# Optimization experiments

Hardware: AMD Instinct MI355X
Metric: run time of the kernel (lower is better)

The kernel has to match this reference:

```python
import jax, jax.numpy as jnp
import numpy as np

LEAK = 0.2

def leaky(x):
    return jnp.where(x > 0, x, LEAK * x)

def relu(x):
    return jnp.maximum(x, 0)

def conv1d(x, w):
    # x [B,Cin,L], w [Cout,Cin,3], stride 1, padding 1
    return jax.lax.conv_general_dilated(x, w, (1,), [(1, 1)],
        dimension_numbers=('NCH', 'OIH', 'NCH'))

def conv2d(x, w, pad, dil=1, groups=1):
    return jax.lax.conv_general_dilated(x, w, (1, 1), [(pad, pad), (pad, pad)],
        rhs_dilation=(dil, dil), feature_group_count=groups,
        dimension_numbers=('NCHW', 'OIHW', 'NCHW'))

def bn2d(x, p, eps=1e-5):
    # p: [4,C] = gamma, beta, running_mean, running_var (eval-mode BN)
    g, b, m, v = p
    s = (1, -1, 1, 1)
    return (x - m.reshape(s)) * (g.reshape(s) / jnp.sqrt(v.reshape(s) + eps)) + b.reshape(s)

def layernorm(x, g, b, eps=1e-5):
    mu = x.mean(-1, keepdims=True)
    var = ((x - mu) ** 2).mean(-1, keepdims=True)
    return (x - mu) / jnp.sqrt(var + eps) * g + b

def l2n(x, axis, eps):
    n = jnp.sqrt((x * x).sum(axis, keepdims=True))
    return x / jnp.maximum(n, eps)


def setup_inputs() -> dict:
    key = jax.random.key(0)
    B, C, H, W = 4, 64, 48, 48
    D, Fn, T, V = 256, 8, 4, 16
    E = 16  # orthogonal prototype embed dim
    ks = iter(jax.random.split(key, 64))
    def rn(shape, s=0.05):
        return jax.random.normal(next(ks), shape, jnp.float32) * s
    def bnp(c):
        return jnp.stack([1.0 + rn((c,), 0.1), rn((c,), 0.1), rn((c,), 0.1), 1.0 + jnp.abs(rn((c,), 0.1))])
    return dict(
        basis_vector_bank=jax.random.normal(next(ks), (T, V, D), jnp.float32),
        task_f=jax.random.normal(next(ks), (B, C, 16, 16), jnp.float32),
        img_f=jax.random.normal(next(ks), (B, C, H, W), jnp.float32),
        protos=jax.random.normal(next(ks), (T, E), jnp.float32),
        tA_w1=rn((E // 4, 1, 3)), tA_w2=rn((E // 2, E // 4, 3)),
        iA_w=rn((E // 2, C, 3, 3)), iA_bn=bnp(E // 2),
        at_w1=rn((E, Fn // 2 * E)), at_b1=rn((Fn // 2 * E,)),
        at_ln_g=jnp.ones((Fn // 2 * E,)), at_ln_b=jnp.zeros((Fn // 2 * E,)),
        at_w2=rn((Fn // 2 * E, Fn * E)), at_b2=rn((Fn * E,)),
        bv_t1=rn((D // 4, 1, 3)), bv_t2=rn((D // 2, D // 4, 3)),
        bv_ic1=rn((D // 4, C, 3, 3)), bv_bn1=bnp(D // 4),
        bv_ic2=rn((D // 2, D // 4, 3, 3)), bv_bn2=bnp(D // 2),
        bv_w1=rn((D, D // 4)), bv_b1=rn((D // 4,)),
        bv_ln_g=jnp.ones((D // 4,)), bv_ln_b=jnp.zeros((D // 4,)),
        bv_w2=rn((D // 4, D)), bv_b2=rn((D,)),
        m1_w1=rn((D, D // 4)), m1_b1=rn((D // 4,)),
        m1_ln_g=jnp.ones((D // 4,)), m1_ln_b=jnp.zeros((D // 4,)),
        m1_w2=rn((D // 4, C * C)), m1_b2=rn((C * C,)),
        m3_w1=rn((D, D // 4)), m3_b1=rn((D // 4,)),
        m3_ln_g=jnp.ones((D // 4,)), m3_ln_b=jnp.zeros((D // 4,)),
        m3_w2=rn((D // 4, 9 * C * C)), m3_b2=rn((9 * C * C,)),
        blr_bn=bnp(C),
        zc_w=rn((C, C, 1, 1), 0.01), zc_b=rn((C,), 0.01),
    )


def _forward(basis_vector_bank, task_f, img_f, protos, tA_w1, tA_w2, iA_w, iA_bn,
             at_w1, at_b1, at_ln_g, at_ln_b, at_w2, at_b2,
             bv_t1, bv_t2, bv_ic1, bv_bn1, bv_ic2, bv_bn2,
             bv_w1, bv_b1, bv_ln_g, bv_ln_b, bv_w2, bv_b2,
             m1_w1, m1_b1, m1_ln_g, m1_ln_b, m1_w2, m1_b2,
             m3_w1, m3_b1, m3_ln_g, m3_ln_b, m3_w2, m3_b2,
             blr_bn, zc_w, zc_b):
    T, V, D = basis_vector_bank.shape
    B, C, H, W = img_f.shape
    E = protos.shape[1]
    Fn = at_w2.shape[1] // E
    tau = 0.5

    # --- A2SI routing features ---
    xt = task_f.reshape(B, 1, -1)
    t1 = conv1d(leaky(conv1d(xt, tA_w1)), tA_w2).mean(-1)          # [B,E/2]
    i1 = leaky(bn2d(conv2d(img_f, iA_w, 1), iA_bn)).mean((2, 3))   # [B,E/2]
    f1 = jnp.concatenate([t1, i1], axis=1)                         # [B,E]
    h = relu(layernorm(f1 @ at_w1 + at_b1, at_ln_g, at_ln_b))
    tif = (h @ at_w2 + at_b2).reshape(B, E, Fn)                    # [B,E,F]
    logits = jnp.einsum('te,bef->bft', l2n(protos, -1, 1e-8), l2n(tif, 1, 1e-8))  # [B,F,T]

    # hard gumbel-softmax (straight-through), fixed noise key for determinism
    u = jax.random.uniform(jax.random.key(42), logits.shape, jnp.float32, 1e-10, 1.0)
    g = -jnp.log(-jnp.log(u))
    y = jax.nn.softmax((logits + g) / tau, axis=-1)
    idx = jnp.argmax(y, axis=-1)                                   # [B,F]
    y_hard = jax.nn.one_hot(idx, T, dtype=y.dtype)
    set_type = y_hard + y - jax.lax.stop_gradient(y)

    bank_flat = basis_vector_bank.reshape(T, V * D)
    sbvb = jnp.einsum('bft,tk->bfk', set_type, bank_flat).reshape(B, Fn, V, D)

    # --- BasisV_filter: filter feature ---
    xt2 = task_f.reshape(B, C, -1)
    rms = jnp.sqrt((xt2 ** 2).mean((1, 2), keepdims=True))
    xt2 = (xt2 / (rms + 1e-8)).reshape(B, 1, -1)
    te = conv1d(leaky(conv1d(xt2, bv_t1)), bv_t2).mean(-1)         # [B,D/2]
    ie = leaky(bn2d(conv2d(img_f, bv_ic1, 1), bv_bn1))
    ie = leaky(bn2d(conv2d(ie, bv_ic2, 1), bv_bn2)).mean((2, 3))   # [B,D/2]
    ff = jnp.concatenate([te, ie], axis=1)                         # [B,D]
    ff = relu(layernorm(ff @ bv_w1 + bv_b1, bv_ln_g, bv_ln_b)) @ bv_w2 + bv_b2

    # --- per-(batch,type) group gather/top-k/scatter, vectorized ---
    # group bank = bank of first filter with that type (hard one-hot -> type's bank)
    occ = idx[:, None, :] == jnp.arange(T)[None, :, None]          # [B,T,F]
    first = jnp.argmax(occ, axis=-1)                               # [B,T]
    Bg = jnp.take_along_axis(sbvb, first[:, :, None, None], axis=1)  # [B,T,V,D]
    # all rows of Q within a group are identical (filter_f expanded over F),
    # so S.max(0) == cosine(ff[b], Bg[b,t])
    scores = jnp.einsum('bd,btvd->btv', l2n(ff, -1, 1e-12), l2n(Bg, -1, 1e-12))
    order = jnp.argsort(-scores, axis=-1)                          # [B,T,V] topk order
    lt = jnp.tril(jnp.ones((Fn, Fn), bool), -1)                    # j < i
    rank = ((idx[:, :, None] == idx[:, None, :]) & lt).sum(-1)     # position in group
    bidx = jnp.arange(B)[:, None]
    sel = order[bidx, idx, rank]                                   # [B,F]
    bvf = Bg[bidx, idx, sel]                                       # [B,F,D]

    # --- per-filter dynamic convolutions ---
    w1 = relu(layernorm(bvf @ m1_w1 + m1_b1, m1_ln_g, m1_ln_b)) @ m1_w2 + m1_b2
    w1 = w1.reshape(B, Fn, C, C)                                   # [B,F,out,in]
    w3 = relu(layernorm(bvf @ m3_w1 + m3_b1, m3_ln_g, m3_ln_b)) @ m3_w2 + m3_b2
    w3 = w3.reshape(B * Fn, C, C, 3, 3)

    dp0 = jnp.einsum('bfoc,bchw->bfohw', w1, img_f)                # 1x1 branch
    xin = jnp.broadcast_to(img_f[:, None], (B, Fn, C, H, W)).reshape(1, B * Fn * C, H, W)
    ker = w3.reshape(B * Fn * C, C, 3, 3)
    dpd = [conv2d(xin, ker, d, dil=d, groups=B * Fn).reshape(B, Fn, C, H, W)
           for d in (1, 2, 3)]                                     # same-padded dilated 3x3
    t_ = idx[:, :, None, None, None]
    dp = jnp.where(t_ == 0, dp0, jnp.where(t_ == 1, dpd[0],
         jnp.where(t_ == 2, dpd[1], dpd[2])))                      # [B,F,C,H,W]

    x = leaky(bn2d(dp.reshape(B * Fn, C, H, W), blr_bn)).reshape(B, Fn, C, H, W).mean(1)
    a = conv2d(x, zc_w, 0) + zc_b.reshape(1, -1, 1, 1)
    return a + img_f


@jax.jit
def reference(basis_vector_bank, task_f, img_f, protos, tA_w1, tA_w2, iA_w, iA_bn,
              at_w1, at_b1, at_ln_g, at_ln_b, at_w2, at_b2,
              bv_t1, bv_t2, bv_ic1, bv_bn1, bv_ic2, bv_bn2,
              bv_w1, bv_b1, bv_ln_g, bv_ln_b, bv_w2, bv_b2,
              m1_w1, m1_b1, m1_ln_g, m1_ln_b, m1_w2, m1_b2,
              m3_w1, m3_b1, m3_ln_g, m3_ln_b, m3_w2, m3_b2,
              blr_bn, zc_w, zc_b):
    return _forward(basis_vector_bank, task_f, img_f, protos, tA_w1, tA_w2, iA_w, iA_bn,
                    at_w1, at_b1, at_ln_g, at_ln_b, at_w2, at_b2,
                    bv_t1, bv_t2, bv_ic1, bv_bn1, bv_ic2, bv_bn2,
                    bv_w1, bv_b1, bv_ln_g, bv_ln_b, bv_w2, bv_b2,
                    m1_w1, m1_b1, m1_ln_g, m1_ln_b, m1_w2, m1_b2,
                    m3_w1, m3_b1, m3_ln_g, m3_ln_b, m3_w2, m3_b2,
                    blr_bn, zc_w, zc_b)
```

## Files before the change

kernel.cpp:

```cpp
#include <hip/hip_runtime.h>
#include <math.h>

#define LEAKC 0.2f

#define NB 4
#define NC 64
#define LLEN 16384
#define HW 2304
#define PP 54
#define PHW 2916
#define SLABP 72
#define CP 72
#define IE1C 50

typedef __attribute__((ext_vector_type(8))) short short8;
typedef __attribute__((ext_vector_type(4))) float floatx4;

__device__ __forceinline__ float leaky(float x){ return x > 0.f ? x : LEAKC*x; }

__device__ __forceinline__ float wave_sum64(float v){
  for(int off=32;off;off>>=1) v += __shfl_xor(v,off);
  return v;
}

__device__ __forceinline__ unsigned short f2bf(float x){
  unsigned u=__float_as_uint(x);
  unsigned r=u+0x7FFFu+((u>>16)&1u);
  return (unsigned short)(r>>16);
}

__device__ __forceinline__ void threefry2x32(unsigned k0, unsigned k1, unsigned& x0, unsigned& x1){
  unsigned ks0=k0, ks1=k1, ks2=k0^k1^0x1BD11BDAu;
  x0+=ks0; x1+=ks1;
  const int rot0[4]={13,15,26,6};
  const int rot1[4]={17,29,16,24};
#define TF_APPLY(rr) {for(int r=0;r<4;r++){x0+=x1; x1=(x1<<rr[r])|(x1>>(32-rr[r])); x1^=x0;}}
  TF_APPLY(rot0); x0+=ks1; x1+=ks2+1u;
  TF_APPLY(rot1); x0+=ks2; x1+=ks0+2u;
  TF_APPLY(rot0); x0+=ks0; x1+=ks1+3u;
  TF_APPLY(rot1); x0+=ks1; x1+=ks2+4u;
  TF_APPLY(rot0); x0+=ks2; x1+=ks0+5u;
#undef TF_APPLY
}

__device__ __forceinline__ float jax_uniform128(int i){
  unsigned x0=0u, x1=(unsigned)i;
  threefry2x32(0u,42u,x0,x1);
  unsigned bits = x0 ^ x1;
  unsigned fb=(bits>>9)|0x3f800000u;
  float f=__uint_as_float(fb)-1.0f;
  float u=f*(1.0f-1e-10f)+1e-10f;
  return fmaxf(1e-10f,u);
}

struct MidSM {
  float sT[64], s0[64], sL[64];
  float red8[64][9];
  float totA_s[4]; float rms_s;
  float part[512];
  float te_s[128], t1_s[8];
  float f1[16], h[64], tif[128], tifn[128], tden[8], pden[4], pn[64], z[32];
  int sidx[8], sfirst[4], srank[8], rows[8];
  float fbuf[256], hh[64], ffn_s[256], finv_s;
  float scores[64];
  int order[64];
  float bvf[2048];
};

__global__ __launch_bounds__(256) void k_pre(const float* __restrict__ task_f,
                      const float* __restrict__ w1A, const float* __restrict__ w1B,
                      float* __restrict__ totApart, float* __restrict__ a0A, float* __restrict__ aLA,
                      float* __restrict__ totBpart, float* __restrict__ a0B, float* __restrict__ aLB,
                      float* __restrict__ rmspart,
                      const float* __restrict__ img,
                      const float* __restrict__ w1, const float* __restrict__ w2,
                      const float* __restrict__ wa,
                      unsigned short* __restrict__ imgTP,
                      unsigned short* __restrict__ W1T, unsigned short* __restrict__ W2T,
                      unsigned short* __restrict__ WAT,
                      const float* __restrict__ mw1, const float* __restrict__ mw3,
                      const float* __restrict__ bvw1p, const float* __restrict__ bvw2p,
                      const float* __restrict__ bvt2p, const float* __restrict__ atw2p,
                      const float* __restrict__ bankp,
                      const float* __restrict__ m1w2p, const float* __restrict__ m3w2p,
                      const float* __restrict__ zcwp,
                      float* __restrict__ warm, int* __restrict__ cnt){
  if(blockIdx.x<256){
    int b=blockIdx.x>>6, seg=blockIdx.x&63;
    const float* x=task_f+b*LLEN;
    float tA[4]={0,0,0,0};
    float tB[64];
#pragma unroll
    for(int c=0;c<64;c++) tB[c]=0.f;
    float sq=0.f;
    int l=seg*256+threadIdx.x;
    {
      float xm=(l>0)?x[l-1]:0.f;
      float xc=x[l];
      float xp=(l<LLEN-1)?x[l+1]:0.f;
      sq=xc*xc;
#pragma unroll
      for(int c=0;c<4;c++){
        float a=leaky(w1A[c*3+0]*xm + w1A[c*3+1]*xc + w1A[c*3+2]*xp);
        tA[c]=a;
        if(l==0) a0A[b*4+c]=a;
        if(l==LLEN-1) aLA[b*4+c]=a;
      }
#pragma unroll
      for(int c=0;c<64;c++){
        float a=leaky(w1B[c*3+0]*xm + w1B[c*3+1]*xc + w1B[c*3+2]*xp);
        tB[c]=a;
        if(l==0) a0B[b*64+c]=a;
        if(l==LLEN-1) aLB[b*64+c]=a;
      }
    }
    sq=wave_sum64(sq);
#pragma unroll
    for(int c=0;c<4;c++) tA[c]=wave_sum64(tA[c]);
#pragma unroll
    for(int c=0;c<64;c++){
      float v=tB[c];
      for(int off=32;off;off>>=1) v+=__shfl_down(v,off);
      tB[c]=v;
    }
    __shared__ float redB[4][64];
    __shared__ float redA[4][4];
    __shared__ float redQ[4];
    int wave=threadIdx.x>>6, lane=threadIdx.x&63;
    if(lane==0){
#pragma unroll
      for(int c=0;c<64;c++) redB[wave][c]=tB[c];
#pragma unroll
      for(int c=0;c<4;c++) redA[wave][c]=tA[c];
      redQ[wave]=sq;
    }
    __syncthreads();
    if(threadIdx.x<64){
      float s=redB[0][threadIdx.x]+redB[1][threadIdx.x]+redB[2][threadIdx.x]+redB[3][threadIdx.x];
      totBpart[(size_t)(b*64+seg)*64+threadIdx.x]=s;
    } else if(threadIdx.x<68){
      int c=threadIdx.x-64;
      totApart[(b*64+seg)*4+c]=redA[0][c]+redA[1][c]+redA[2][c]+redA[3][c];
    } else if(threadIdx.x==68){
      rmspart[b*64+seg]=redQ[0]+redQ[1]+redQ[2]+redQ[3];
    }
  } else if(blockIdx.x<400){
    int blk=blockIdx.x-256;
    int b=blk/36, t=blk%36;
    int p0=t*64;
    __shared__ float tile[64][65];
    int pp=threadIdx.x&63, c4=threadIdx.x>>6;
    for(int r=0;r<16;r++){
      int c=c4*16+r;
      tile[c][pp]=img[(b*64+c)*HW + p0+pp];
    }
    __syncthreads();
    int pxl=threadIdx.x>>2, cg=(threadIdx.x&3)*16;
    unsigned out[8];
#pragma unroll
    for(int q=0;q<8;q++){
      unsigned lo=f2bf(tile[cg+2*q][pxl]);
      unsigned hi=f2bf(tile[cg+2*q+1][pxl]);
      out[q]=lo|(hi<<16);
    }
    int px=p0+pxl;
    int h=px/48, w=px-h*48;
    int poff=(h+3)*PP+(w+3);
    unsigned* dst=(unsigned*)(imgTP + ((size_t)(b*PHW+poff))*64 + cg);
#pragma unroll
    for(int q=0;q<8;q++) dst[q]=out[q];
  } else if(blockIdx.x<868){
    int n=(blockIdx.x-400)*256+threadIdx.x;
    if(n<9*64*64){
      int tap=n>>12, oc=(n>>6)&63, c=n&63;
      W1T[n]=f2bf(w1[oc*576+c*9+tap]);
    } else if(n<9*64*64+9*128*64){
      int m=n-9*64*64;
      int tap=m/8192, r=m-tap*8192, oc=r>>6, c=r&63;
      W2T[m]=f2bf(w2[oc*576+c*9+tap]);
    } else {
      int q=n-9*64*64-9*128*64;
      if(q<9*16*64){
        int tap=q>>10, r=q&1023, o=r>>6, c=r&63;
        WAT[q]=(o<8)?f2bf(wa[o*576+c*9+tap]):(unsigned short)0;
      }
    }
  } else if(blockIdx.x<932){
    int t=(blockIdx.x-868)*256+threadIdx.x;
    float a=0.f;
    for(int i=t;i*16<16384;i+=16384) a+=mw1[i*16];
    for(int i=t;i*16<16384;i+=16384) a+=mw3[i*16];
    for(int i=t;i*16<16384;i+=16384) a+=bvw1p[i*16];
    for(int i=t;i*16<16384;i+=16384) a+=bvw2p[i*16];
    for(int i=t;i*16<24576;i+=16384) a+=bvt2p[i*16];
    for(int i=t;i*16<8192;i+=16384) a+=atw2p[i*16];
    for(int i=t;i*16<16384;i+=16384) a+=bankp[i*16];
    for(int i=t;i*16<262144;i+=16384) a+=m1w2p[i*16];
    for(int i=t;i*16<2359296;i+=16384) a+=m3w2p[i*16];
    for(int i=t;i*16<4096;i+=16384) a+=zcwp[i*16];
    warm[t&1023]=a;
  } else {
    if(blockIdx.x==932 && threadIdx.x<4)
      __hip_atomic_store(&cnt[threadIdx.x],0,__ATOMIC_RELAXED,__HIP_MEMORY_SCOPE_AGENT);
    int id=(blockIdx.x-932)*256+threadIdx.x;
    uint4 z=make_uint4(0,0,0,0);
    for(int cch=id;cch<19584;cch+=4096){
      int ck=cch&7, pxid=cch>>3;
      int b=pxid/612, p=pxid-b*612;
      int h,w;
      if(p<324){ int r=p/54; w=p-r*54; h=(r<3)?r:(r+48); }
      else { int q=p-324; int r2=q/6; int cc=q-r2*6; h=3+r2; w=(cc<3)?cc:(cc+48); }
      *(uint4*)(imgTP + ((size_t)(b*PHW + h*PP + w))*64 + ck*8)=z;
    }
  }
}

__global__ __launch_bounds__(512) void k_cm(const unsigned short* __restrict__ imgTP,
    const unsigned short* __restrict__ W1T, const unsigned short* __restrict__ W2T,
    const unsigned short* __restrict__ WAT,
    const float* __restrict__ bn1, const float* __restrict__ bn2, const float* __restrict__ bnA,
    float* __restrict__ iepart, float* __restrict__ i1part,
    const float* __restrict__ totApart, const float* __restrict__ a0A, const float* __restrict__ aLA,
    const float* __restrict__ totBpart, const float* __restrict__ a0B, const float* __restrict__ aLB,
    const float* __restrict__ rmspart,
    const float* __restrict__ tA_w2, const float* __restrict__ bv_t2,
    const float* __restrict__ at_w1, const float* __restrict__ at_b1,
    const float* __restrict__ at_ln_g, const float* __restrict__ at_ln_b,
    const float* __restrict__ at_w2, const float* __restrict__ at_b2,
    const float* __restrict__ protos,
    const float* __restrict__ bv_w1, const float* __restrict__ bv_b1,
    const float* __restrict__ bv_ln_g, const float* __restrict__ bv_ln_b,
    const float* __restrict__ bv_w2, const float* __restrict__ bv_b2,
    const float* __restrict__ bank,
    const float* __restrict__ m1_w1, const float* __restrict__ m1_b1,
    const float* __restrict__ m1_g,  const float* __restrict__ m1_bb,
    const float* __restrict__ m3_w1, const float* __restrict__ m3_b1,
    const float* __restrict__ m3_g,  const float* __restrict__ m3_bb,
    int* __restrict__ idxo, float* __restrict__ hid1, float* __restrict__ hid3,
    int* __restrict__ cnt){
  __shared__ __align__(16) char smraw[75456];
  int tid=threadIdx.x;
  int lane=tid&63, wv=tid>>6;
  int n0=lane&15, kg=lane>>4;
  if(blockIdx.x<96){
    int blk=blockIdx.x;
    int b=blk/24, hp=blk-b*24;
    int h0=hp*2;
    unsigned short* slab=(unsigned short*)smraw;
    unsigned short* ie1=(unsigned short*)(smraw+46656);
    {
      const unsigned short* ibase=imgTP+((size_t)b*PHW+(size_t)(h0+1)*PP)*64;
      for(int e=tid;e<6*54*8;e+=512){
        int rr=e/(54*8), rem=e-rr*54*8, w=rem>>3, ck=rem&7;
        uint4 v=*(const uint4*)(ibase+((size_t)(rr*PP+w))*64+ck*8);
        *(uint4*)(slab+(rr*54+w)*SLABP+ck*8)=v;
      }
      if(tid<64){
        int br=tid>>4, cq=(tid>>3)&1, ck=tid&7;
        *(uint4*)(ie1+((size_t)(br*IE1C+(cq?49:0)))*CP+ck*8)=make_uint4(0,0,0,0);
      }
    }
    __syncthreads();
    {
      int mt=wv&3, rh=wv>>2;
      floatx4 acc[2][3];
#pragma unroll
      for(int rr=0;rr<2;rr++)
#pragma unroll
        for(int nt=0;nt<3;nt++) acc[rr][nt]=(floatx4){0.f,0.f,0.f,0.f};
#pragma unroll
      for(int ti=0;ti<3;ti++){
#pragma unroll
        for(int tj=0;tj<3;tj++){
          int tap=ti*3+tj;
          const unsigned short* Ab=W1T+(size_t)tap*4096;
#pragma unroll
          for(int c0=0;c0<64;c0+=32){
            short8 a=*(const short8*)(Ab+((mt*16+n0)*64+c0+kg*8));
#pragma unroll
            for(int rr=0;rr<2;rr++){
              int sr=rh*2+rr+ti;
#pragma unroll
              for(int nt=0;nt<3;nt++){
                int sc=nt*16+n0+tj+2;
                short8 bv=*(const short8*)(slab+(sr*54+sc)*SLABP+c0+kg*8);
                acc[rr][nt]=__builtin_amdgcn_mfma_f32_16x16x32_bf16(a,bv,acc[rr][nt],0,0,0);
              }
            }
          }
        }
      }
      int obase=mt*16+kg*4;
      float scale[4],m_[4],be_[4];
#pragma unroll
      for(int reg=0;reg<4;reg++){
        int o=obase+reg;
        scale[reg]=bn1[o]/sqrtf(bn1[192+o]+1e-5f);
        m_[reg]=bn1[128+o]; be_[reg]=bn1[64+o];
      }
#pragma unroll
      for(int rr=0;rr<2;rr++){
        int br=rh*2+rr;
        bool rv=((unsigned)(h0-1+br))<48u;
#pragma unroll
        for(int nt=0;nt<3;nt++){
          float v0=rv?leaky((acc[rr][nt][0]-m_[0])*scale[0]+be_[0]):0.f;
          float v1=rv?leaky((acc[rr][nt][1]-m_[1])*scale[1]+be_[1]):0.f;
          float v2=rv?leaky((acc[rr][nt][2]-m_[2])*scale[2]+be_[2]):0.f;
          float v3=rv?leaky((acc[rr][nt][3]-m_[3])*scale[3]+be_[3]):0.f;
          unsigned w0=f2bf(v0)|((unsigned)f2bf(v1)<<16);
          unsigned w1=f2bf(v2)|((unsigned)f2bf(v3)<<16);
          uint2 pk={w0,w1};
          *(uint2*)(ie1+((size_t)(br*IE1C+(nt*16+1+n0)))*CP+obase)=pk;
        }
      }
    }
    __syncthreads();
    {
      int mt2=wv;
      floatx4 acc[6];
#pragma unroll
      for(int i=0;i<6;i++) acc[i]=(floatx4){0.f,0.f,0.f,0.f};
#pragma unroll
      for(int ti=0;ti<3;ti++){
#pragma unroll
        for(int tj=0;tj<3;tj++){
          int tap=ti*3+tj;
          const unsigned short* Ab=W2T+(size_t)tap*8192;
#pragma unroll
          for(int c0=0;c0<64;c0+=32){
            short8 a=*(const short8*)(Ab+((mt2*16+n0)*64+c0+kg*8));
#pragma unroll
            for(int rr=0;rr<2;rr++){
              int sr=rr+ti;
#pragma unroll
              for(int wc=0;wc<3;wc++){
                int q=wc*16+n0+tj;
                short8 bv=*(const short8*)(ie1+((size_t)(sr*IE1C+q))*CP+c0+kg*8);
                acc[rr*3+wc]=__builtin_amdgcn_mfma_f32_16x16x32_bf16(a,bv,acc[rr*3+wc],0,0,0);
              }
            }
          }
        }
      }
      int obase=mt2*16+kg*4;
#pragma unroll
      for(int reg=0;reg<4;reg++){
        int o=obase+reg;
        float scale=bn2[o]/sqrtf(bn2[384+o]+1e-5f);
        float m_=bn2[256+o], be_=bn2[128+o];
        float part=0;
#pragma unroll
        for(int i=0;i<6;i++) part+=leaky((acc[i][reg]-m_)*scale+be_);
        for(int off=1;off<16;off<<=1) part+=__shfl_xor(part,off);
        if(n0==0) iepart[(b*24+hp)*128+o]=part*(1.f/2304.f);
      }
    }
    __syncthreads();
    if(tid==0) __hip_atomic_fetch_add(&cnt[0],1,__ATOMIC_RELEASE,__HIP_MEMORY_SCOPE_AGENT);
  } else if(blockIdx.x<108){
    int blk2=blockIdx.x-96;
    int b=blk2/3, hg=blk2%3;
    int hp=hg*8+wv;
    int h0=hp*2;
    const unsigned short* ib=imgTP+(size_t)b*PHW*64;
    floatx4 acc[6];
#pragma unroll
    for(int i=0;i<6;i++) acc[i]=(floatx4){0.f,0.f,0.f,0.f};
#pragma unroll
    for(int ti=0;ti<3;ti++){
#pragma unroll
      for(int tj=0;tj<3;tj++){
        int tap=ti*3+tj;
        const unsigned short* Ab=WAT+(size_t)tap*1024;
#pragma unroll
        for(int c0=0;c0<64;c0+=32){
          short8 a=*(const short8*)(Ab+(n0*64+c0+kg*8));
#pragma unroll
          for(int rr=0;rr<2;rr++){
            int r=h0+rr+ti-1+3;
#pragma unroll
            for(int wc=0;wc<3;wc++){
              int w=wc*16+n0+tj-1+3;
              short8 bv=*(const short8*)(ib+((size_t)(r*PP+w)*64+c0+kg*8));
              acc[rr*3+wc]=__builtin_amdgcn_mfma_f32_16x16x32_bf16(a,bv,acc[rr*3+wc],0,0,0);
            }
          }
        }
      }
    }
    int obase=kg*4;
#pragma unroll
    for(int reg=0;reg<4;reg++){
      int o=obase+reg;
      float part=0;
      if(o<8){
        float scale=bnA[o]/sqrtf(bnA[24+o]+1e-5f);
        float m_=bnA[16+o], be_=bnA[8+o];
#pragma unroll
        for(int i=0;i<6;i++) part+=leaky((acc[i][reg]-m_)*scale+be_);
      }
      for(int off=1;off<16;off<<=1) part+=__shfl_xor(part,off);
      if(n0==0 && o<8) i1part[(b*24+hp)*8+o]=part*(1.f/2304.f);
    }
    __syncthreads();
    if(tid==0) __hip_atomic_fetch_add(&cnt[1],1,__ATOMIC_RELEASE,__HIP_MEMORY_SCOPE_AGENT);
  } else {
    MidSM* S=(MidSM*)smraw;
    int b=blockIdx.x-108;
    const float invL=1.0f/16384.0f;
    {
      int c8=tid>>3, g8=tid&7;
      float s8=0;
#pragma unroll
      for(int seg=g8*8;seg<g8*8+8;seg++) s8+=totBpart[(size_t)(b*64+seg)*64+c8];
      S->red8[c8][g8]=s8;
    }
    if(tid>=64 && tid<128){
      int t=tid-64;
      S->s0[t]=a0B[b*64+t]; S->sL[t]=aLB[b*64+t];
    } else if(tid>=128 && tid<192){
      float v=rmspart[b*64+(tid-128)];
      v=wave_sum64(v);
      if(tid==128) S->rms_s=v;
    } else if(tid>=192 && tid<196){
      int c=tid-192;
      float s=0;
#pragma unroll 8
      for(int seg=0;seg<64;seg++) s+=totApart[(b*64+seg)*4+c];
      S->totA_s[c]=s;
    }
    __syncthreads();
    if(tid<64){
      float s=0;
#pragma unroll
      for(int g=0;g<8;g++) s+=S->red8[tid][g];
      S->sT[tid]=s;
    }
    __syncthreads();
    float scB=1.0f/(sqrtf(S->rms_s*invL)+1e-8f);
    if(tid<256){
      int c2=tid&127, h2=tid>>7;
      const float* wr=bv_t2+c2*192;
      float s=0;
      for(int c1=h2*32;c1<h2*32+32;c1+=8){
        float4 q[6];
        const float4* r4=(const float4*)(wr+c1*3);
#pragma unroll
        for(int u=0;u<6;u++) q[u]=r4[u];
        const float* qq=(const float*)q;
#pragma unroll
        for(int u=0;u<8;u++){
          int c=c1+u;
          float T=S->sT[c], A0=S->s0[c], AL=S->sL[c];
          s += qq[u*3+0]*(T-AL) + qq[u*3+1]*T + qq[u*3+2]*(T-A0);
        }
      }
      S->part[tid]=s;
    } else if(tid>=384 && tid<392){
      int c2=tid-384;
      float s=0;
      for(int c1=0;c1<4;c1++){
        float T=S->totA_s[c1], A0=a0A[b*4+c1], AL=aLA[b*4+c1];
        const float* w=&tA_w2[(c2*4+c1)*3];
        s += w[0]*(T-AL) + w[1]*T + w[2]*(T-A0);
      }
      S->t1_s[c2]=s*invL;
    }
    __syncthreads();
    if(tid<128) S->te_s[tid]=(S->part[tid]+S->part[tid+128])*invL*scB;
    __syncthreads();
    if(tid==0){
      while(__hip_atomic_load(&cnt[1],__ATOMIC_ACQUIRE,__HIP_MEMORY_SCOPE_AGENT)<12)
        __builtin_amdgcn_s_sleep(8);
    }
    __syncthreads();
    if(tid<8) S->f1[tid]=S->t1_s[tid];
    else if(tid<16){
      int f=tid-8;
      float s=0;
#pragma unroll
      for(int g=0;g<24;g++) s+=i1part[(b*24+g)*8+f];
      S->f1[tid]=s;
    }
    __syncthreads();
    if(tid<64){
      float s=at_b1[lane];
#pragma unroll
      for(int i=0;i<16;i++) s+=S->f1[i]*at_w1[i*64+lane];
      float mu=wave_sum64(s)*(1.f/64.f);
      float d=s-mu;
      float var=wave_sum64(d*d)*(1.f/64.f);
      S->h[lane]=fmaxf(d*(1.0f/sqrtf(var+1e-5f))*at_ln_g[lane]+at_ln_b[lane],0.f);
    }
    __syncthreads();
    if(tid<256){
      int n=tid&127, h2=tid>>7;
      float a0=0,a1=0;
      for(int k=h2*32;k<h2*32+32;k+=2){
        a0+=S->h[k]*at_w2[k*128+n];
        a1+=S->h[k+1]*at_w2[(k+1)*128+n];
      }
      S->part[tid]=a0+a1;
    }
    __syncthreads();
    if(tid<128) S->tif[tid]=at_b2[tid]+S->part[tid]+S->part[tid+128];
    __syncthreads();
    if(tid<8){
      int f=tid;
      float ss=0; for(int e=0;e<16;e++){float v=S->tif[e*8+f]; ss+=v*v;}
      S->tden[f]=fmaxf(sqrtf(ss),1e-8f);
    } else if(tid<12){
      int t=tid-8;
      float ss=0; for(int e=0;e<16;e++){float v=protos[t*16+e]; ss+=v*v;}
      S->pden[t]=fmaxf(sqrtf(ss),1e-8f);
    }
    __syncthreads();
    if(tid<128) S->tifn[tid]=S->tif[tid]/S->tden[tid&7];
    if(tid<64) S->pn[tid]=protos[tid]/S->pden[tid>>4];
    __syncthreads();
    if(tid<32){
      int f=tid>>2, t=tid&3;
      float ss=0;
#pragma unroll
      for(int e=0;e<16;e++) ss+=S->pn[t*16+e]*S->tifn[e*8+f];
      float u=jax_uniform128(b*32+f*4+t);
      float g=-logf(-logf(u));
      S->z[tid]=ss+g;
    }
    __syncthreads();
    if(tid<8){
      float best=S->z[tid*4]; int bi=0;
      for(int t=1;t<4;t++){ float v=S->z[tid*4+t]; if(v>best){best=v;bi=t;} }
      S->sidx[tid]=bi;
    }
    __syncthreads();
    if(tid<4){
      int t=tid;
      int fi=0;
      for(int f=7;f>=0;f--) if(S->sidx[f]==t) fi=f;
      S->sfirst[t]=fi;
    } else if(tid<12){
      int f=tid-4;
      int c=0; for(int f2=0;f2<f;f2++) if(S->sidx[f2]==S->sidx[f]) c++;
      S->srank[f]=c;
    }
    __syncthreads();
    if(tid==0){
      while(__hip_atomic_load(&cnt[0],__ATOMIC_ACQUIRE,__HIP_MEMORY_SCOPE_AGENT)<96)
        __builtin_amdgcn_s_sleep(8);
    }
    __syncthreads();
    if(tid<128) S->fbuf[tid]=S->te_s[tid];
    else if(tid<256){
      int c=tid-128;
      float s=0;
#pragma unroll 8
      for(int g=0;g<24;g++) s+=iepart[(b*24+g)*128+c];
      S->fbuf[tid]=s;
    }
    __syncthreads();
    if(tid<256){
      int l64=tid&63, q=tid>>6;
      float a0=0,a1=0,a2=0,a3=0;
      for(int k=q*64;k<q*64+64;k+=4){
        a0+=S->fbuf[k]  *bv_w1[k*64+l64];
        a1+=S->fbuf[k+1]*bv_w1[(k+1)*64+l64];
        a2+=S->fbuf[k+2]*bv_w1[(k+2)*64+l64];
        a3+=S->fbuf[k+3]*bv_w1[(k+3)*64+l64];
      }
      S->part[tid]=((a0+a1)+(a2+a3));
    }
    __syncthreads();
    if(tid<64){
      float s=bv_b1[lane]+S->part[lane]+S->part[64+lane]+S->part[128+lane]+S->part[192+lane];
      float mu=wave_sum64(s)*(1.f/64.f);
      float d=s-mu;
      float var=wave_sum64(d*d)*(1.f/64.f);
      S->hh[lane]=fmaxf(d*(1.0f/sqrtf(var+1e-5f))*bv_ln_g[lane]+bv_ln_b[lane],0.f);
    }
    __syncthreads();
    {
      int n=tid&255, h2=tid>>8;
      float a0=0,a1=0;
      for(int k=h2*32;k<h2*32+32;k+=2){
        a0+=S->hh[k]*bv_w2[k*256+n];
        a1+=S->hh[k+1]*bv_w2[(k+1)*256+n];
      }
      S->part[tid]=a0+a1;
    }
    __syncthreads();
    if(tid<256) S->ffn_s[tid]=bv_b2[tid]+S->part[tid]+S->part[tid+256];
    __syncthreads();
    if(tid<64){
      float sq=0;
#pragma unroll
      for(int u=0;u<4;u++){ float v=S->ffn_s[u*64+lane]; sq+=v*v; }
      sq=wave_sum64(sq);
      if(lane==0) S->finv_s=1.0f/fmaxf(sqrtf(sq),1e-12f);
    }
    __syncthreads();
    if(tid<256) S->ffn_s[tid]*=S->finv_s;
    __syncthreads();

    if(tid<128){
      int it=tid&63, h2=tid>>6;
      int t=it>>4, v=it&15;
      int tt=S->sidx[S->sfirst[t]];
      const float4* row=(const float4*)(bank+(tt*16+v)*256);
      float sa=0,na=0;
      for(int d4=h2*32;d4<h2*32+32;d4++){
        float4 r=row[d4];
        const float* fp=&S->ffn_s[d4*4];
        sa+=fp[0]*r.x+fp[1]*r.y+fp[2]*r.z+fp[3]*r.w;
        na+=r.x*r.x+r.y*r.y+r.z*r.z+r.w*r.w;
      }
      S->part[tid]=sa;
      S->part[256+tid]=na;
    }
    __syncthreads();
    if(tid<64) S->scores[tid]=(S->part[tid]+S->part[tid+64])/fmaxf(sqrtf(S->part[256+tid]+S->part[320+tid]),1e-12f);
    __syncthreads();
    if(tid<4){
      const float* sc=&S->scores[tid*16];
      unsigned used=0;
      for(int pk=0;pk<16;pk++){
        int best=-1; float bv=-1e30f;
        for(int v2=0;v2<16;v2++){
          if(used&(1u<<v2)) continue;
          float vv=sc[v2];
          if(best<0||vv>bv){bv=vv;best=v2;}
        }
        used|=1u<<best;
        S->order[tid*16+pk]=best;
      }
    }
    __syncthreads();
    if(tid<8){
      int t=S->sidx[tid];
      int v=S->order[t*16+S->srank[tid]];
      S->rows[tid]=t*16+v;
      idxo[b*8+tid]=t;
    }
    __syncthreads();

    for(int ii=tid;ii<2048;ii+=512){
      int r=ii>>8, d=ii&255;
      S->bvf[ii]=bank[S->rows[r]*256+d];
    }
    __syncthreads();
    {
      int r=wv;
      const float* bp=&S->bvf[r*256];
      float a0=0,a1=0,a2=0,a3=0;
      float c0=0,c1=0,c2=0,c3=0;
      for(int d=0;d<256;d+=4){
        float b0=bp[d],b1=bp[d+1],b2=bp[d+2],b3=bp[d+3];
        a0+=b0*m1_w1[d*64+lane];
        a1+=b1*m1_w1[(d+1)*64+lane];
        a2+=b2*m1_w1[(d+2)*64+lane];
        a3+=b3*m1_w1[(d+3)*64+lane];
        c0+=b0*m3_w1[d*64+lane];
        c1+=b1*m3_w1[(d+1)*64+lane];
        c2+=b2*m3_w1[(d+2)*64+lane];
        c3+=b3*m3_w1[(d+3)*64+lane];
      }
      float s1=m1_b1[lane]+((a0+a1)+(a2+a3));
      float s3=m3_b1[lane]+((c0+c1)+(c2+c3));
      float mu=wave_sum64(s1)*(1.f/64.f);
      float dd=s1-mu;
      float var=wave_sum64(dd*dd)*(1.f/64.f);
      hid1[(b*8+r)*64+lane]=fmaxf(dd*(1.0f/sqrtf(var+1e-5f))*m1_g[lane]+m1_bb[lane],0.f);
      mu=wave_sum64(s3)*(1.f/64.f);
      dd=s3-mu;
      var=wave_sum64(dd*dd)*(1.f/64.f);
      hid3[(b*8+r)*64+lane]=fmaxf(dd*(1.0f/sqrtf(var+1e-5f))*m3_g[lane]+m3_bb[lane],0.f);
    }
  }
}

__global__ __launch_bounds__(256) void k_heads(const float* __restrict__ hid1, const float* __restrict__ hid3,
                        const float* __restrict__ w2a, const float* __restrict__ b2a,
                        const float* __restrict__ w2b, const float* __restrict__ b2b,
                        unsigned short* __restrict__ A1, unsigned short* __restrict__ A3){
  __shared__ float hl[2048];
  if(blockIdx.x<16){
    int n=blockIdx.x*256+threadIdx.x;
    float wcol[64];
#pragma unroll
    for(int k=0;k<64;k++) wcol[k]=w2a[k*4096+n];
    float bb=b2a[n];
    for(int i=threadIdx.x;i<2048;i+=256) hl[i]=hid1[i];
    __syncthreads();
    for(int bf=0;bf<32;bf++){
      float s=bb;
#pragma unroll
      for(int k=0;k<64;k++) s+=hl[bf*64+k]*wcol[k];
      A1[bf*4096+n]=f2bf(s);
    }
  } else {
    int n=(blockIdx.x-16)*256+threadIdx.x;
    float wcol[64];
#pragma unroll
    for(int k=0;k<64;k++) wcol[k]=w2b[(size_t)k*36864+n];
    float bb=b2b[n];
    for(int i=threadIdx.x;i<2048;i+=256) hl[i]=hid3[i];
    __syncthreads();
    int o=n/576, rem=n-o*576;
    int c=rem/9, tap=rem-c*9;
    size_t base=((size_t)tap*64+o)*64+c;
    for(int bf=0;bf<32;bf++){
      float s=bb;
#pragma unroll
      for(int k=0;k<64;k++) s+=hl[bf*64+k]*wcol[k];
      A3[(size_t)bf*9*4096+base]=f2bf(s);
    }
  }
}

__global__ __launch_bounds__(512) void k_dynF(const unsigned short* __restrict__ imgTP,
                       const unsigned short* __restrict__ A1, const unsigned short* __restrict__ A3,
                       const int* __restrict__ idx, const float* __restrict__ bn,
                       const float* __restrict__ zc_w, const float* __restrict__ zc_b,
                       const float* __restrict__ img, float* __restrict__ out){
  int blk=blockIdx.x;
  int b=blk/48, r0=blk-b*48;
  int tid=threadIdx.x;
  int lane=tid&63, w8=tid>>6;
  int mt=w8&3, fh=w8>>2;
  int n0=lane&15, kg=lane>>4;
  __shared__ unsigned short slab[7*54*SLABP];
  __shared__ float xl[64*50];
  __shared__ float zl[4096];
  int tts[4];
#pragma unroll
  for(int i=0;i<4;i++) tts[i]=idx[b*8+fh*4+i];
  int obase=mt*16+kg*4;
  float scale[4],m_[4],be_[4];
#pragma unroll
  for(int reg=0;reg<4;reg++){
    int o=obase+reg;
    scale[reg]=bn[o]/sqrtf(bn[192+o]+1e-5f);
    m_[reg]=bn[128+o]; be_[reg]=bn[64+o];
  }
  for(int i=tid;i<4096;i+=512) zl[i]=zc_w[i];
  for(int i=tid;i<3200;i+=512) xl[i]=0.f;
  {
    const unsigned short* ibase=imgTP+((size_t)b*PHW+(size_t)r0*PP)*64;
    for(int e=tid;e<7*54*8;e+=512){
      int rr=e/(54*8), rem=e-rr*54*8, w=rem>>3, ck=rem&7;
      uint4 v=*(const uint4*)(ibase + ((size_t)(rr*PP+w))*64 + ck*8);
      *(uint4*)(slab + (rr*54+w)*SLABP + ck*8)=v;
    }
  }
  __syncthreads();
  float xsum[3][4];
#pragma unroll
  for(int wc=0;wc<3;wc++)
#pragma unroll
    for(int reg=0;reg<4;reg++) xsum[wc][reg]=0.f;
#pragma unroll
  for(int fi=0;fi<4;fi++){
    int f=fh*4+fi;
    int bf=b*8+f;
    int tt=tts[fi];
    floatx4 acc[3];
#pragma unroll
    for(int i=0;i<3;i++) acc[i]=(floatx4){0.f,0.f,0.f,0.f};
    if(tt==0){
      const unsigned short* Ab=A1+(size_t)bf*4096;
#pragma unroll
      for(int c0=0;c0<64;c0+=32){
        short8 a=*(const short8*)(Ab+((mt*16+n0)*64+c0+kg*8));
#pragma unroll
        for(int wc=0;wc<3;wc++){
          short8 bv=*(const short8*)(slab + (3*54 + wc*16+n0+3)*SLABP + c0+kg*8);
          acc[wc]=__builtin_amdgcn_mfma_f32_16x16x32_bf16(a,bv,acc[wc],0,0,0);
        }
      }
    } else {
      int d=tt;
      const unsigned short* A3b=A3+(size_t)bf*9*4096;
#pragma unroll
      for(int ti=0;ti<3;ti++){
        int lr=d*(ti-1)+3;
#pragma unroll
        for(int tj=0;tj<3;tj++){
          int tap=ti*3+tj;
          int dw=d*(tj-1)+3;
          const unsigned short* Ab=A3b+(size_t)tap*4096;
#pragma unroll
          for(int c0=0;c0<64;c0+=32){
            short8 a=*(const short8*)(Ab+((mt*16+n0)*64+c0+kg*8));
#pragma unroll
            for(int wc=0;wc<3;wc++){
              short8 bv=*(const short8*)(slab + (lr*54 + wc*16+n0+dw)*SLABP + c0+kg*8);
              acc[wc]=__builtin_amdgcn_mfma_f32_16x16x32_bf16(a,bv,acc[wc],0,0,0);
            }
          }
        }
      }
    }
#pragma unroll
    for(int wc=0;wc<3;wc++)
#pragma unroll
      for(int reg=0;reg<4;reg++)
        xsum[wc][reg]+=leaky((acc[wc][reg]-m_[reg])*scale[reg]+be_[reg]);
  }
#pragma unroll
  for(int wc=0;wc<3;wc++)
#pragma unroll
    for(int reg=0;reg<4;reg++)
      atomicAdd(&xl[(obase+reg)*50 + wc*16+n0], xsum[wc][reg]*0.125f);
  __syncthreads();
  size_t base=(size_t)b*64*HW + r0*48;
  for(int e=tid;e<3072;e+=512){
    int o=e/48, px=e-o*48;
    float s=zc_b[o];
#pragma unroll
    for(int c=0;c<64;c++) s+=zl[o*64+c]*xl[c*50+px];
    size_t a=base+(size_t)o*HW+px;
    out[a]=s+img[a];
  }
}

extern "C" void kernel_launch(void* const* d_in, const int* in_sizes, int n_in,
                              void* d_out, int out_size, void* d_ws, size_t ws_size,
                              hipStream_t stream){
  const float* bank   =(const float*)d_in[0];
  const float* task_f =(const float*)d_in[1];
  const float* img_f  =(const float*)d_in[2];
  const float* protos =(const float*)d_in[3];
  const float* tA_w1  =(const float*)d_in[4];
  const float* tA_w2  =(const float*)d_in[5];
  const float* iA_w   =(const float*)d_in[6];
  const float* iA_bn  =(const float*)d_in[7];
  const float* at_w1  =(const float*)d_in[8];
  const float* at_b1  =(const float*)d_in[9];
  const float* at_ln_g=(const float*)d_in[10];
  const float* at_ln_b=(const float*)d_in[11];
  const float* at_w2  =(const float*)d_in[12];
  const float* at_b2  =(const float*)d_in[13];
  const float* bv_t1  =(const float*)d_in[14];
  const float* bv_t2  =(const float*)d_in[15];
  const float* bv_ic1 =(const float*)d_in[16];
  const float* bv_bn1 =(const float*)d_in[17];
  const float* bv_ic2 =(const float*)d_in[18];
  const float* bv_bn2 =(const float*)d_in[19];
  const float* bv_w1  =(const float*)d_in[20];
  const float* bv_b1  =(const float*)d_in[21];
  const float* bv_ln_g=(const float*)d_in[22];
  const float* bv_ln_b=(const float*)d_in[23];
  const float* bv_w2  =(const float*)d_in[24];
  const float* bv_b2  =(const float*)d_in[25];
  const float* m1_w1  =(const float*)d_in[26];
  const float* m1_b1  =(const float*)d_in[27];
  const float* m1_ln_g=(const float*)d_in[28];
  const float* m1_ln_b=(const float*)d_in[29];
  const float* m1_w2  =(const float*)d_in[30];
  const float* m1_b2  =(const float*)d_in[31];
  const float* m3_w1  =(const float*)d_in[32];
  const float* m3_b1  =(const float*)d_in[33];
  const float* m3_ln_g=(const float*)d_in[34];
  const float* m3_ln_b=(const float*)d_in[35];
  const float* m3_w2  =(const float*)d_in[36];
  const float* m3_b2  =(const float*)d_in[37];
  const float* blr_bn =(const float*)d_in[38];
  const float* zc_w   =(const float*)d_in[39];
  const float* zc_b   =(const float*)d_in[40];

  float* ws=(float*)d_ws;
  float* totApart=ws+0;
  float* a0A  =ws+1024;
  float* aLA  =ws+1040;
  float* totBpart=ws+1056;
  float* a0B  =ws+17440;
  float* aLB  =ws+17696;
  float* rmspart=ws+17952;
  float* i1part =ws+18208;
  float* iepart =ws+18976;
  int*   idxp   =(int*)(ws+31264);
  float* hid1=ws+31296;
  float* hid3=ws+33344;
  unsigned short* A1p  =(unsigned short*)(ws+35392);
  unsigned short* A3p  =(unsigned short*)(ws+100928);
  unsigned short* imgTP=(unsigned short*)(ws+690752);
  unsigned short* W1Tp =(unsigned short*)(ws+1064000);
  unsigned short* W2Tp =(unsigned short*)(ws+1082432);
  unsigned short* WATp =(unsigned short*)(ws+1119296);
  float* warm =ws+1123904;
  int*   cnt  =(int*)(ws+1124928);

  k_pre<<<948,256,0,stream>>>(task_f, tA_w1, bv_t1,
                              totApart, a0A, aLA, totBpart, a0B, aLB, rmspart,
                              img_f, bv_ic1, bv_ic2, iA_w, imgTP, W1Tp, W2Tp, WATp,
                              m1_w1, m3_w1, bv_w1, bv_w2, bv_t2, at_w2, bank,
                              m1_w2, m3_w2, zc_w, warm, cnt);
  k_cm<<<112,512,0,stream>>>(imgTP, W1Tp, W2Tp, WATp, bv_bn1, bv_bn2, iA_bn,
                             iepart, i1part,
                             totApart, a0A, aLA, totBpart, a0B, aLB, rmspart,
                             tA_w2, bv_t2,
                             at_w1, at_b1, at_ln_g, at_ln_b, at_w2, at_b2, protos,
                             bv_w1, bv_b1, bv_ln_g, bv_ln_b, bv_w2, bv_b2, bank,
                             m1_w1, m1_b1, m1_ln_g, m1_ln_b,
                             m3_w1, m3_b1, m3_ln_g, m3_ln_b,
                             idxp, hid1, hid3, cnt);
  k_heads<<<160,256,0,stream>>>(hid1, hid3, m1_w2, m1_b2, m3_w2, m3_b2, A1p, A3p);
  k_dynF<<<192,512,0,stream>>>(imgTP, A1p, A3p, idxp, blr_bn, zc_w, zc_b, img_f, (float*)d_out);

  (void)in_sizes; (void)n_in; (void)out_size; (void)ws_size;
}
```

Before: 266.6 us.

## Move MLP first-layer into k_heads, spread over 64 blocks with atomic handoff

The per-batch first hidden layer (bank row gather, 256x64 matvec, layernorm, ReLU) moves out of the tail of the few k_cm blocks and into 64 extra k_heads blocks, each handling one row and one head with the K dimension split across four waves. The second-layer blocks load their weight columns first, then spin on an agent-scope atomic counter until all hidden rows are written. The goal is to shorten the serial critical path at the end of k_cm and overlap it with the weight loads. The cost is spin-wait coupling between blocks, which assumes every block is co-resident, and the counter must be reset for each call.

```diff
diff --git a/kernel.cpp b/kernel.cpp
--- a/kernel.cpp
+++ b/kernel.cpp
@@ -60,11 +60,10 @@
   float part[512];
   float te_s[128], t1_s[8];
   float f1[16], h[64], tif[128], tifn[128], tden[8], pden[4], pn[64], z[32];
-  int sidx[8], sfirst[4], srank[8], rows[8];
+  int sidx[8], sfirst[4], srank[8];
   float fbuf[256], hh[64], ffn_s[256], finv_s;
   float scores[64];
   int order[64];
-  float bvf[2048];
 };
 
 __global__ __launch_bounds__(256) void k_pre(const float* __restrict__ task_f,
@@ -232,11 +231,7 @@
     const float* __restrict__ bv_ln_g, const float* __restrict__ bv_ln_b,
     const float* __restrict__ bv_w2, const float* __restrict__ bv_b2,
     const float* __restrict__ bank,
-    const float* __restrict__ m1_w1, const float* __restrict__ m1_b1,
-    const float* __restrict__ m1_g,  const float* __restrict__ m1_bb,
-    const float* __restrict__ m3_w1, const float* __restrict__ m3_b1,
-    const float* __restrict__ m3_g,  const float* __restrict__ m3_bb,
-    int* __restrict__ idxo, float* __restrict__ hid1, float* __restrict__ hid3,
+    int* __restrict__ idxo, int* __restrict__ rowsp,
     int* __restrict__ cnt){
   __shared__ __align__(16) char smraw[75456];
   int tid=threadIdx.x;
@@ -639,72 +634,90 @@
     if(tid<8){
       int t=S->sidx[tid];
       int v=S->order[t*16+S->srank[tid]];
-      S->rows[tid]=t*16+v;
+      rowsp[b*8+tid]=t*16+v;
       idxo[b*8+tid]=t;
-    }
-    __syncthreads();
-
-    for(int ii=tid;ii<2048;ii+=512){
-      int r=ii>>8, d=ii&255;
-      S->bvf[ii]=bank[S->rows[r]*256+d];
-    }
-    __syncthreads();
-    {
-      int r=wv;
-      const float* bp=&S->bvf[r*256];
-      float a0=0,a1=0,a2=0,a3=0;
-      float c0=0,c1=0,c2=0,c3=0;
-      for(int d=0;d<256;d+=4){
-        float b0=bp[d],b1=bp[d+1],b2=bp[d+2],b3=bp[d+3];
-        a0+=b0*m1_w1[d*64+lane];
-        a1+=b1*m1_w1[(d+1)*64+lane];
-        a2+=b2*m1_w1[(d+2)*64+lane];
-        a3+=b3*m1_w1[(d+3)*64+lane];
-        c0+=b0*m3_w1[d*64+lane];
-        c1+=b1*m3_w1[(d+1)*64+lane];
-        c2+=b2*m3_w1[(d+2)*64+lane];
-        c3+=b3*m3_w1[(d+3)*64+lane];
-      }
-      float s1=m1_b1[lane]+((a0+a1)+(a2+a3));
-      float s3=m3_b1[lane]+((c0+c1)+(c2+c3));
-      float mu=wave_sum64(s1)*(1.f/64.f);
-      float dd=s1-mu;
-      float var=wave_sum64(dd*dd)*(1.f/64.f);
-      hid1[(b*8+r)*64+lane]=fmaxf(dd*(1.0f/sqrtf(var+1e-5f))*m1_g[lane]+m1_bb[lane],0.f);
-      mu=wave_sum64(s3)*(1.f/64.f);
-      dd=s3-mu;
-      var=wave_sum64(dd*dd)*(1.f/64.f);
-      hid3[(b*8+r)*64+lane]=fmaxf(dd*(1.0f/sqrtf(var+1e-5f))*m3_g[lane]+m3_bb[lane],0.f);
     }
   }
 }
 
-__global__ __launch_bounds__(256) void k_heads(const float* __restrict__ hid1, const float* __restrict__ hid3,
-                        const float* __restrict__ w2a, const float* __restrict__ b2a,
-                        const float* __restrict__ w2b, const float* __restrict__ b2b,
-                        unsigned short* __restrict__ A1, unsigned short* __restrict__ A3){
-  __shared__ float hl[2048];
-  if(blockIdx.x<16){
-    int n=blockIdx.x*256+threadIdx.x;
+__global__ __launch_bounds__(256) void k_heads(
+    const float* __restrict__ bank, const int* __restrict__ rowsp,
+    const float* __restrict__ m1_w1, const float* __restrict__ m1_b1,
+    const float* __restrict__ m1_g,  const float* __restrict__ m1_bb,
+    const float* __restrict__ m3_w1, const float* __restrict__ m3_b1,
+    const float* __restrict__ m3_g,  const float* __restrict__ m3_bb,
+    float* __restrict__ hid1, float* __restrict__ hid3,
+    const float* __restrict__ w2a, const float* __restrict__ b2a,
+    const float* __restrict__ w2b, const float* __restrict__ b2b,
+    unsigned short* __restrict__ A1, unsigned short* __restrict__ A3,
+    int* __restrict__ cnt){
+  __shared__ float sm[2048];
+  int tid=threadIdx.x;
+  if(blockIdx.x<64){
+    float* row=sm;
+    float (*red)[64]=(float(*)[64])(sm+256);
+    int chunk=blockIdx.x;
+    int m=chunk&1, br=chunk>>1;
+    int lane=tid&63, q=tid>>6;
+    if(tid<64){
+      float4 v=((const float4*)(bank+(size_t)rowsp[br]*256))[tid];
+      ((float4*)row)[tid]=v;
+    }
+    __syncthreads();
+    const float* w=m?m3_w1:m1_w1;
+    float a0=0,a1=0,a2=0,a3=0;
+    for(int d=q*64;d<q*64+64;d+=4){
+      a0+=row[d]  *w[(size_t)d*64+lane];
+      a1+=row[d+1]*w[(size_t)(d+1)*64+lane];
+      a2+=row[d+2]*w[(size_t)(d+2)*64+lane];
+      a3+=row[d+3]*w[(size_t)(d+3)*64+lane];
+    }
+    red[q][lane]=((a0+a1)+(a2+a3));
+    __syncthreads();
+    if(tid<64){
+      const float* b1=m?m3_b1:m1_b1;
+      const float* g =m?m3_g :m1_g;
+      const float* bb=m?m3_bb:m1_bb;
+      float s=b1[lane]+red[0][lane]+red[1][lane]+red[2][lane]+red[3][lane];
+      float mu=wave_sum64(s)*(1.f/64.f);
+      float d=s-mu;
+      float var=wave_sum64(d*d)*(1.f/64.f);
+      float* hid=m?hid3:hid1;
+      hid[br*64+lane]=fmaxf(d*(1.0f/sqrtf(var+1e-5f))*g[lane]+bb[lane],0.f);
+    }
+    __syncthreads();
+    if(tid==0) __hip_atomic_fetch_add(&cnt[3],1,__ATOMIC_RELEASE,__HIP_MEMORY_SCOPE_AGENT);
+  } else if(blockIdx.x<80){
+    int n=(blockIdx.x-64)*256+tid;
     float wcol[64];
 #pragma unroll
     for(int k=0;k<64;k++) wcol[k]=w2a[k*4096+n];
     float bb=b2a[n];
-    for(int i=threadIdx.x;i<2048;i+=256) hl[i]=hid1[i];
+    if(tid==0){
+      while(__hip_atomic_load(&cnt[3],__ATOMIC_ACQUIRE,__HIP_MEMORY_SCOPE_AGENT)<64)
+        __builtin_amdgcn_s_sleep(8);
+    }
+    __syncthreads();
+    for(int i=tid;i<2048;i+=256) sm[i]=hid1[i];
     __syncthreads();
     for(int bf=0;bf<32;bf++){
       float s=bb;
 #pragma unroll
-      for(int k=0;k<64;k++) s+=hl[bf*64+k]*wcol[k];
+      for(int k=0;k<64;k++) s+=sm[bf*64+k]*wcol[k];
       A1[bf*4096+n]=f2bf(s);
     }
   } else {
-    int n=(blockIdx.x-16)*256+threadIdx.x;
+    int n=(blockIdx.x-80)*256+tid;
     float wcol[64];
 #pragma unroll
     for(int k=0;k<64;k++) wcol[k]=w2b[(size_t)k*36864+n];
     float bb=b2b[n];
-    for(int i=threadIdx.x;i<2048;i+=256) hl[i]=hid3[i];
+    if(tid==0){
+      while(__hip_atomic_load(&cnt[3],__ATOMIC_ACQUIRE,__HIP_MEMORY_SCOPE_AGENT)<64)
+        __builtin_amdgcn_s_sleep(8);
+    }
+    __syncthreads();
+    for(int i=tid;i<2048;i+=256) sm[i]=hid3[i];
     __syncthreads();
     int o=n/576, rem=n-o*576;
     int c=rem/9, tap=rem-c*9;
@@ -712,7 +725,7 @@
     for(int bf=0;bf<32;bf++){
       float s=bb;
 #pragma unroll
-      for(int k=0;k<64;k++) s+=hl[bf*64+k]*wcol[k];
+      for(int k=0;k<64;k++) s+=sm[bf*64+k]*wcol[k];
       A3[(size_t)bf*9*4096+base]=f2bf(s);
     }
   }
@@ -880,16 +893,17 @@
   float* i1part =ws+18208;
   float* iepart =ws+18976;
   int*   idxp   =(int*)(ws+31264);
-  float* hid1=ws+31296;
-  float* hid3=ws+33344;
-  unsigned short* A1p  =(unsigned short*)(ws+35392);
-  unsigned short* A3p  =(unsigned short*)(ws+100928);
-  unsigned short* imgTP=(unsigned short*)(ws+690752);
-  unsigned short* W1Tp =(unsigned short*)(ws+1064000);
-  unsigned short* W2Tp =(unsigned short*)(ws+1082432);
-  unsigned short* WATp =(unsigned short*)(ws+1119296);
-  float* warm =ws+1123904;
-  int*   cnt  =(int*)(ws+1124928);
+  int*   rowsp  =(int*)(ws+31296);
+  float* hid1=ws+31328;
+  float* hid3=ws+33376;
+  unsigned short* A1p  =(unsigned short*)(ws+35424);
+  unsigned short* A3p  =(unsigned short*)(ws+100960);
+  unsigned short* imgTP=(unsigned short*)(ws+690784);
+  unsigned short* W1Tp =(unsigned short*)(ws+1064032);
+  unsigned short* W2Tp =(unsigned short*)(ws+1082464);
+  unsigned short* WATp =(unsigned short*)(ws+1119328);
+  float* warm =ws+1123936;
+  int*   cnt  =(int*)(ws+1124960);
 
   k_pre<<<948,256,0,stream>>>(task_f, tA_w1, bv_t1,
                               totApart, a0A, aLA, totBpart, a0B, aLB, rmspart,
@@ -902,10 +916,12 @@
                              tA_w2, bv_t2,
                              at_w1, at_b1, at_ln_g, at_ln_b, at_w2, at_b2, protos,
                              bv_w1, bv_b1, bv_ln_g, bv_ln_b, bv_w2, bv_b2, bank,
-                             m1_w1, m1_b1, m1_ln_g, m1_ln_b,
-                             m3_w1, m3_b1, m3_ln_g, m3_ln_b,
-                             idxp, hid1, hid3, cnt);
-  k_heads<<<160,256,0,stream>>>(hid1, hid3, m1_w2, m1_b2, m3_w2, m3_b2, A1p, A3p);
+                             idxp, rowsp, cnt);
+  k_heads<<<224,256,0,stream>>>(bank, rowsp,
+                                m1_w1, m1_b1, m1_ln_g, m1_ln_b,
+                                m3_w1, m3_b1, m3_ln_g, m3_ln_b,
+                                hid1, hid3,
+                                m1_w2, m1_b2, m3_w2, m3_b2, A1p, A3p, cnt);
   k_dynF<<<192,512,0,stream>>>(imgTP, A1p, A3p, idxp, blr_bn, zc_w, zc_b, img_f, (float*)d_out);
 
   (void)in_sizes; (void)n_in; (void)out_size; (void)ws_size;
```

Result: no change. 269.2 us (+1.0%).
